# Kernel tuning notes

Measured on AMD Instinct MI355X. Metric: run time of the kernel, lower is better.

Reference implementation:

```python
import jax, jax.numpy as jnp
import numpy as np

TOKENS, D_MODEL, D_FF, RANK = 16384, 1024, 2816, 16


def setup_inputs() -> dict:
    key = jax.random.key(0)
    ks = jax.random.split(key, 7)
    s = lambda k, shp, scale: jax.random.normal(k, shp, dtype=jnp.float32) * scale
    return {
        "x": s(ks[0], (TOKENS, D_MODEL), 1.0),
        "W_gate_up": s(ks[1], (D_MODEL, 2 * D_FF), 0.02),
        "A_gate_up": s(ks[2], (D_MODEL, RANK), 0.02),
        "B_gate_up": s(ks[3], (RANK, 2 * D_FF), 0.02),
        "W_down": s(ks[4], (D_FF, D_MODEL), 0.02),
        "A_down": s(ks[5], (D_FF, RANK), 0.02),
        "B_down": s(ks[6], (RANK, D_MODEL), 0.02),
    }


def reference(x, W_gate_up, A_gate_up, B_gate_up, W_down, A_down, B_down):
    # gate_up_proj: base GEMM + LoRA low-rank correction
    gate_up = x @ W_gate_up + (x @ A_gate_up) @ B_gate_up  # [T, 2*D_FF]
    gate, up = jnp.split(gate_up, 2, axis=-1)
    h = jax.nn.silu(gate) * up  # SiluAndMul, [T, D_FF]
    # down_proj: base GEMM + LoRA correction
    out = h @ W_down + (h @ A_down) @ B_down  # [T, D_MODEL]
    return out
```

## Files before the change

### kernel.cpp

```cpp
#include <hip/hip_runtime.h>


typedef __bf16 bf16_t;
typedef __bf16 bf16x4 __attribute__((ext_vector_type(4)));
typedef __bf16 bf16x8 __attribute__((ext_vector_type(8)));
typedef float f32x4 __attribute__((ext_vector_type(4)));

#define TOKENS 16384
#define DMODEL 1024
#define DFF    2816
#define N2F    5632

#define BARM() asm volatile("s_barrier" ::: "memory")
#define VMW(n) asm volatile("s_waitcnt vmcnt(" #n ")" ::: "memory")
#define MFMA(d, va, vb) d = __builtin_amdgcn_mfma_f32_16x16x32_bf16(va, vb, d, 0, 0, 0)

__device__ __forceinline__ void gload16(const bf16_t* g, bf16_t* l) {
    __builtin_amdgcn_global_load_lds(
        (const __attribute__((address_space(1))) void*)g,
        (__attribute__((address_space(3))) void*)l, 16, 0, 0);
}

template<int KTOT, int NTOT>
__global__ __launch_bounds__(256) void prep_weff(
        const float* __restrict__ W, const float* __restrict__ A,
        const float* __restrict__ B, bf16_t* __restrict__ Wt) {
    __shared__ float Ws[64][65];
    __shared__ float As[64][17];
    __shared__ float Bs[16][64];
    const int t = threadIdx.x;
    const int k0 = blockIdx.x * 64, n0 = blockIdx.y * 64;
    #pragma unroll
    for (int i = 0; i < 16; ++i) {
        int row = i * 4 + t / 64, col = t % 64;
        Ws[row][col] = W[(size_t)(k0 + row) * NTOT + n0 + col];
    }
    #pragma unroll
    for (int i = 0; i < 4; ++i) {
        int idx = i * 256 + t;
        As[idx / 16][idx % 16] = A[(size_t)(k0 + idx / 16) * 16 + idx % 16];
    }
    #pragma unroll
    for (int i = 0; i < 4; ++i) {
        int idx = i * 256 + t;
        Bs[idx / 64][idx % 64] = B[(size_t)(idx / 64) * NTOT + n0 + idx % 64];
    }
    __syncthreads();
    const int kl = t % 64;
    #pragma unroll
    for (int j = 0; j < 16; ++j) {
        int nl = j * 4 + t / 64;
        float val = Ws[kl][nl];
        #pragma unroll
        for (int r = 0; r < 16; ++r) val += As[kl][r] * Bs[r][nl];
        Wt[(size_t)(n0 + nl) * KTOT + k0 + kl] = (bf16_t)val;
    }
}

__global__ __launch_bounds__(256) void conv_bf16(
        const float* __restrict__ in, bf16_t* __restrict__ out, int n4) {
    int i = blockIdx.x * 256 + threadIdx.x;
    if (i < n4) {
        float4 v = ((const float4*)in)[i];
        bf16x4 o;
        o.x = (bf16_t)v.x; o.y = (bf16_t)v.y; o.z = (bf16_t)v.z; o.w = (bf16_t)v.w;
        ((bf16x4*)out)[i] = o;
    }
}

__global__ __launch_bounds__(512, 2) void gemm1(
        const bf16_t* __restrict__ X, const bf16_t* __restrict__ Wt,
        bf16_t* __restrict__ H) {
    __shared__ bf16_t lds[65536];
    const int t = threadIdx.x, l = t & 63;
    const int wid = t >> 6, wr = wid >> 2, wc = wid & 3;
    const int l15 = l & 15, lhi = l >> 4;
    const int wg = ((int)blockIdx.x & 7) * 176 + ((int)blockIdx.x >> 3);
    const int tf = wg >> 6, tm = wg & 63;
    const int mbase = tm * 256, fbase = tf * 128;
    const int srow = t >> 2;
    const int sc8 = (((t & 3) ^ (srow & 3))) * 8;
    const bf16_t* gA  = X  + (size_t)(mbase + srow) * DMODEL + sc8;
    const bf16_t* gBg = Wt + (size_t)(fbase + srow) * DMODEL + sc8;
    const bf16_t* gBu = Wt + (size_t)(DFF + fbase + srow) * DMODEL + sc8;
    bf16_t* sdA = lds + wid * 512;
    bf16_t* sdB = lds + 16384 + wid * 512;
    const int aoff = (wr * 128 + l15) * 32 + (lhi ^ (l15 & 3)) * 8;
    const int boff = 16384 + (wc * 32 + l15) * 32 + (lhi ^ (l15 & 3)) * 8;

    f32x4 accg[8][2] = {}, accu[8][2] = {};
    bf16x8 a[4], bg[2], bu[2];

#define G1_STAGE_A(kt, ks, buf) do { const int kc = (kt) * 64 + (ks) * 32;        \
    gload16(gA + kc, sdA + (buf) * 32768 + (ks) * 8192);                          \
    gload16(gA + (size_t)128 * DMODEL + kc,                                       \
            sdA + (buf) * 32768 + (ks) * 8192 + 4096); } while (0)
#define G1_STAGE_B(kt, ks, buf) do { const int kc = (kt) * 64 + (ks) * 32;        \
    gload16(gBg + kc, sdB + (buf) * 32768 + (ks) * 8192);                         \
    gload16(gBu + kc, sdB + (buf) * 32768 + (ks) * 8192 + 4096); } while (0)
#define G1_READ_A(mh, ks, cur) do {                                               \
    const bf16_t* p = lds + (cur) * 32768 + (ks) * 8192 + (mh) * 2048 + aoff;     \
    a[0] = *(const bf16x8*)(p);        a[1] = *(const bf16x8*)(p + 512);          \
    a[2] = *(const bf16x8*)(p + 1024); a[3] = *(const bf16x8*)(p + 1536); } while (0)
#define G1_READ_B(ks, cur) do {                                                   \
    const bf16_t* p = lds + (cur) * 32768 + (ks) * 8192 + boff;                   \
    bg[0] = *(const bf16x8*)(p);        bg[1] = *(const bf16x8*)(p + 512);        \
    bu[0] = *(const bf16x8*)(p + 4096); bu[1] = *(const bf16x8*)(p + 4608); } while (0)
#define G1_MFMA(mh) do { __builtin_amdgcn_s_setprio(1);                           \
    _Pragma("unroll")                                                             \
    for (int i = 0; i < 4; ++i) {                                                 \
        MFMA(accg[(mh) * 4 + i][0], a[i], bg[0]);                                 \
        MFMA(accu[(mh) * 4 + i][0], a[i], bu[0]);                                 \
        MFMA(accg[(mh) * 4 + i][1], a[i], bg[1]);                                 \
        MFMA(accu[(mh) * 4 + i][1], a[i], bu[1]);                                 \
    }                                                                             \
    __builtin_amdgcn_s_setprio(0); } while (0)

    G1_STAGE_A(0, 0, 0); G1_STAGE_B(0, 0, 0); G1_STAGE_A(0, 1, 0); G1_STAGE_B(0, 1, 0);
    G1_STAGE_B(1, 0, 1); G1_STAGE_A(1, 0, 1); G1_STAGE_B(1, 1, 1);
    VMW(6); BARM();

    const int NT = DMODEL / 64;
    for (int kt = 0; kt < NT; ++kt) {
        const int cur = kt & 1, nxt = cur ^ 1;
        if (kt + 1 < NT) G1_STAGE_A(kt + 1, 1, nxt);
        G1_READ_A(0, 0, cur); G1_READ_B(0, cur);
        BARM();
        G1_MFMA(0);
        BARM();
        if (kt + 2 < NT) G1_STAGE_B(kt + 2, 0, cur);
        G1_READ_A(1, 0, cur);
        BARM();
        G1_MFMA(1);
        BARM();
        if (kt + 2 < NT) G1_STAGE_A(kt + 2, 0, cur);
        G1_READ_A(0, 1, cur); G1_READ_B(1, cur);
        BARM();
        G1_MFMA(0);
        BARM();
        if (kt + 2 < NT) G1_STAGE_B(kt + 2, 1, cur);
        G1_READ_A(1, 1, cur);
        if (kt + 2 < NT) { VMW(6); } else { VMW(0); }
        BARM();
        G1_MFMA(1);
        BARM();
    }
#undef G1_STAGE_A
#undef G1_STAGE_B
#undef G1_READ_A
#undef G1_READ_B
#undef G1_MFMA

    #pragma unroll
    for (int m = 0; m < 8; ++m)
        #pragma unroll
        for (int n = 0; n < 2; ++n)
            #pragma unroll
            for (int r = 0; r < 4; ++r) {
                int row = mbase + wr * 128 + m * 16 + lhi * 4 + r;
                int col = fbase + wc * 32 + n * 16 + l15;
                float g = accg[m][n][r], u = accu[m][n][r];
                H[(size_t)row * DFF + col] = (bf16_t)(g / (1.0f + __expf(-g)) * u);
            }
}

__global__ __launch_bounds__(512, 2) void gemm2(
        const bf16_t* __restrict__ Hm, const bf16_t* __restrict__ Wt,
        float* __restrict__ O) {
    __shared__ bf16_t lds[65536];
    const int t = threadIdx.x, l = t & 63;
    const int wid = t >> 6, wr = wid >> 2, wc = wid & 3;
    const int l15 = l & 15, lhi = l >> 4;
    const int wg = ((int)blockIdx.x & 7) * 32 + ((int)blockIdx.x >> 3);
    const int tn = wg >> 6, tm = wg & 63;
    const int mbase = tm * 256, nbase = tn * 256;
    const int srow = t >> 2;
    const int sc8 = (((t & 3) ^ (srow & 3))) * 8;
    const bf16_t* gA = Hm + (size_t)(mbase + srow) * DFF + sc8;
    const bf16_t* gB = Wt + (size_t)(nbase + srow) * DFF + sc8;
    bf16_t* sdA = lds + wid * 512;
    bf16_t* sdB = lds + 16384 + wid * 512;
    const int aoff = (wr * 128 + l15) * 32 + (lhi ^ (l15 & 3)) * 8;
    const int boff = 16384 + (wc * 64 + l15) * 32 + (lhi ^ (l15 & 3)) * 8;

    f32x4 acc[8][4] = {};
    bf16x8 a[4], b[4];

#define G2_STAGE_A(kt, ks, buf) do { const int kc = (kt) * 64 + (ks) * 32;        \
    gload16(gA + kc, sdA + (buf) * 32768 + (ks) * 8192);                          \
    gload16(gA + (size_t)128 * DFF + kc,                                          \
            sdA + (buf) * 32768 + (ks) * 8192 + 4096); } while (0)
#define G2_STAGE_B(kt, ks, buf) do { const int kc = (kt) * 64 + (ks) * 32;        \
    gload16(gB + kc, sdB + (buf) * 32768 + (ks) * 8192);                          \
    gload16(gB + (size_t)128 * DFF + kc,                                          \
            sdB + (buf) * 32768 + (ks) * 8192 + 4096); } while (0)
#define G2_READ_A(mh, ks, cur) do {                                               \
    const bf16_t* p = lds + (cur) * 32768 + (ks) * 8192 + (mh) * 2048 + aoff;     \
    a[0] = *(const bf16x8*)(p);        a[1] = *(const bf16x8*)(p + 512);          \
    a[2] = *(const bf16x8*)(p + 1024); a[3] = *(const bf16x8*)(p + 1536); } while (0)
#define G2_READ_B(ks, cur) do {                                                   \
    const bf16_t* p = lds + (cur) * 32768 + (ks) * 8192 + boff;                   \
    b[0] = *(const bf16x8*)(p);        b[1] = *(const bf16x8*)(p + 512);          \
    b[2] = *(const bf16x8*)(p + 1024); b[3] = *(const bf16x8*)(p + 1536); } while (0)
#define G2_MFMA(mh) do { __builtin_amdgcn_s_setprio(1);                           \
    _Pragma("unroll")                                                             \
    for (int i = 0; i < 4; ++i) {                                                 \
        MFMA(acc[(mh) * 4 + i][0], a[i], b[0]);                                   \
        MFMA(acc[(mh) * 4 + i][1], a[i], b[1]);                                   \
        MFMA(acc[(mh) * 4 + i][2], a[i], b[2]);                                   \
        MFMA(acc[(mh) * 4 + i][3], a[i], b[3]);                                   \
    }                                                                             \
    __builtin_amdgcn_s_setprio(0); } while (0)

    G2_STAGE_A(0, 0, 0); G2_STAGE_B(0, 0, 0); G2_STAGE_A(0, 1, 0); G2_STAGE_B(0, 1, 0);
    G2_STAGE_B(1, 0, 1); G2_STAGE_A(1, 0, 1); G2_STAGE_B(1, 1, 1);
    VMW(6); BARM();

    const int NT = DFF / 64;
    for (int kt = 0; kt < NT; ++kt) {
        const int cur = kt & 1, nxt = cur ^ 1;
        if (kt + 1 < NT) G2_STAGE_A(kt + 1, 1, nxt);
        G2_READ_A(0, 0, cur); G2_READ_B(0, cur);
        BARM();
        G2_MFMA(0);
        BARM();
        if (kt + 2 < NT) G2_STAGE_B(kt + 2, 0, cur);
        G2_READ_A(1, 0, cur);
        BARM();
        G2_MFMA(1);
        BARM();
        if (kt + 2 < NT) G2_STAGE_A(kt + 2, 0, cur);
        G2_READ_A(0, 1, cur); G2_READ_B(1, cur);
        BARM();
        G2_MFMA(0);
        BARM();
        if (kt + 2 < NT) G2_STAGE_B(kt + 2, 1, cur);
        G2_READ_A(1, 1, cur);
        if (kt + 2 < NT) { VMW(6); } else { VMW(0); }
        BARM();
        G2_MFMA(1);
        BARM();
    }
#undef G2_STAGE_A
#undef G2_STAGE_B
#undef G2_READ_A
#undef G2_READ_B
#undef G2_MFMA

    #pragma unroll
    for (int m = 0; m < 8; ++m)
        #pragma unroll
        for (int n = 0; n < 4; ++n)
            #pragma unroll
            for (int r = 0; r < 4; ++r) {
                int row = mbase + wr * 128 + m * 16 + lhi * 4 + r;
                int col = nbase + wc * 64 + n * 16 + l15;
                O[(size_t)row * DMODEL + col] = acc[m][n][r];
            }
}

extern "C" void kernel_launch(void* const* d_in, const int* in_sizes, int n_in,
                              void* d_out, int out_size, void* d_ws, size_t ws_size,
                              hipStream_t stream) {
    const float* x   = (const float*)d_in[0];
    const float* Wgu = (const float*)d_in[1];
    const float* Agu = (const float*)d_in[2];
    const float* Bgu = (const float*)d_in[3];
    const float* Wd  = (const float*)d_in[4];
    const float* Ad  = (const float*)d_in[5];
    const float* Bd  = (const float*)d_in[6];
    float* out = (float*)d_out;
    char* ws = (char*)d_ws;

    bf16_t* wgut = (bf16_t*)(ws);
    bf16_t* wdt  = (bf16_t*)(ws + 11534336);
    bf16_t* xb   = (bf16_t*)(ws + 17301504);
    bf16_t* hb   = (bf16_t*)(ws + 50855936);

    prep_weff<DMODEL, N2F><<<dim3(DMODEL / 64, N2F / 64), 256, 0, stream>>>(
        Wgu, Agu, Bgu, wgut);
    prep_weff<DFF, DMODEL><<<dim3(DFF / 64, DMODEL / 64), 256, 0, stream>>>(
        Wd, Ad, Bd, wdt);
    conv_bf16<<<(TOKENS * DMODEL / 4) / 256, 256, 0, stream>>>(
        x, xb, TOKENS * DMODEL / 4);
    gemm1<<<22 * 64, 512, 0, stream>>>(xb, wgut, hb);
    gemm2<<<4 * 64, 512, 0, stream>>>(hb, wdt, out);
}
```

Baseline: 369.8 us.

## Shrink GEMM tiles and switch to triple-buffered single-barrier K pipeline

Both GEMMs move from 256x128 (gemm1) and 256x256 (gemm2) tiles with a double-buffered, 64-wide K step and eight barriers per iteration to half-width tiles with a 32-wide K step, three LDS buffers and two barriers per iteration. LDS per block drops and launch bounds rise to 4 blocks per CU, which doubles the grid and aims for more occupancy and better latency hiding. The trade-off is lower arithmetic intensity per tile: there are fewer MFMAs per LDS read and more global traffic for re-reading the shared operand.

After: 411.4 us. +11.2%, slower.

```diff
diff --git a/kernel.cpp b/kernel.cpp
--- a/kernel.cpp
+++ b/kernel.cpp
@@ -68,192 +68,149 @@
     }
 }
 
-__global__ __launch_bounds__(512, 2) void gemm1(
+__global__ __launch_bounds__(512, 4) void gemm1(
         const bf16_t* __restrict__ X, const bf16_t* __restrict__ Wt,
         bf16_t* __restrict__ H) {
-    __shared__ bf16_t lds[65536];
+    __shared__ bf16_t lds[36864];
     const int t = threadIdx.x, l = t & 63;
-    const int wid = t >> 6, wr = wid >> 2, wc = wid & 3;
+    const int wid = t >> 6, wr = wid >> 1, wc = wid & 1;
     const int l15 = l & 15, lhi = l >> 4;
-    const int wg = ((int)blockIdx.x & 7) * 176 + ((int)blockIdx.x >> 3);
+    const int wg = ((int)blockIdx.x & 7) * 352 + ((int)blockIdx.x >> 3);
     const int tf = wg >> 6, tm = wg & 63;
-    const int mbase = tm * 256, fbase = tf * 128;
+    const int mbase = tm * 256, fbase = tf * 64;
     const int srow = t >> 2;
-    const int sc8 = (((t & 3) ^ (srow & 3))) * 8;
-    const bf16_t* gA  = X  + (size_t)(mbase + srow) * DMODEL + sc8;
-    const bf16_t* gBg = Wt + (size_t)(fbase + srow) * DMODEL + sc8;
-    const bf16_t* gBu = Wt + (size_t)(DFF + fbase + srow) * DMODEL + sc8;
+    const int sc8 = ((t & 3) ^ (srow & 3)) * 8;
+    const bf16_t* gA  = X + (size_t)(mbase + srow) * DMODEL + sc8;
+    const bf16_t* gA2 = gA + (size_t)128 * DMODEL;
+    const int brow = (srow < 64) ? (fbase + srow) : (DFF + fbase + srow - 64);
+    const bf16_t* gB  = Wt + (size_t)brow * DMODEL + sc8;
     bf16_t* sdA = lds + wid * 512;
-    bf16_t* sdB = lds + 16384 + wid * 512;
-    const int aoff = (wr * 128 + l15) * 32 + (lhi ^ (l15 & 3)) * 8;
-    const int boff = 16384 + (wc * 32 + l15) * 32 + (lhi ^ (l15 & 3)) * 8;
-
-    f32x4 accg[8][2] = {}, accu[8][2] = {};
+    bf16_t* sdB = lds + 8192 + wid * 512;
+    const int rsw = (lhi ^ (l15 & 3)) * 8;
+    const int aoff = (wr * 64 + l15) * 32 + rsw;
+    const int boff = 8192 + (wc * 32 + l15) * 32 + rsw;
+
+    f32x4 accg[4][2] = {}, accu[4][2] = {};
     bf16x8 a[4], bg[2], bu[2];
 
-#define G1_STAGE_A(kt, ks, buf) do { const int kc = (kt) * 64 + (ks) * 32;        \
-    gload16(gA + kc, sdA + (buf) * 32768 + (ks) * 8192);                          \
-    gload16(gA + (size_t)128 * DMODEL + kc,                                       \
-            sdA + (buf) * 32768 + (ks) * 8192 + 4096); } while (0)
-#define G1_STAGE_B(kt, ks, buf) do { const int kc = (kt) * 64 + (ks) * 32;        \
-    gload16(gBg + kc, sdB + (buf) * 32768 + (ks) * 8192);                         \
-    gload16(gBu + kc, sdB + (buf) * 32768 + (ks) * 8192 + 4096); } while (0)
-#define G1_READ_A(mh, ks, cur) do {                                               \
-    const bf16_t* p = lds + (cur) * 32768 + (ks) * 8192 + (mh) * 2048 + aoff;     \
+#define G1_STAGE(kt, buf) do { const int kc = (kt) * 32;                          \
+    bf16_t* d = (buf) * 12288 + sdA;                                              \
+    gload16(gA + kc, d); gload16(gA2 + kc, d + 4096);                             \
+    gload16(gB + kc, (buf) * 12288 + sdB); } while (0)
+#define G1_READ(buf) do {                                                         \
+    const bf16_t* p = lds + (buf) * 12288 + aoff;                                 \
     a[0] = *(const bf16x8*)(p);        a[1] = *(const bf16x8*)(p + 512);          \
-    a[2] = *(const bf16x8*)(p + 1024); a[3] = *(const bf16x8*)(p + 1536); } while (0)
-#define G1_READ_B(ks, cur) do {                                                   \
-    const bf16_t* p = lds + (cur) * 32768 + (ks) * 8192 + boff;                   \
-    bg[0] = *(const bf16x8*)(p);        bg[1] = *(const bf16x8*)(p + 512);        \
-    bu[0] = *(const bf16x8*)(p + 4096); bu[1] = *(const bf16x8*)(p + 4608); } while (0)
-#define G1_MFMA(mh) do { __builtin_amdgcn_s_setprio(1);                           \
+    a[2] = *(const bf16x8*)(p + 1024); a[3] = *(const bf16x8*)(p + 1536);         \
+    const bf16_t* q = lds + (buf) * 12288 + boff;                                 \
+    bg[0] = *(const bf16x8*)(q);        bg[1] = *(const bf16x8*)(q + 512);        \
+    bu[0] = *(const bf16x8*)(q + 2048); bu[1] = *(const bf16x8*)(q + 2560); } while (0)
+#define G1_MFMA() do { __builtin_amdgcn_s_setprio(1);                             \
     _Pragma("unroll")                                                             \
     for (int i = 0; i < 4; ++i) {                                                 \
-        MFMA(accg[(mh) * 4 + i][0], a[i], bg[0]);                                 \
-        MFMA(accu[(mh) * 4 + i][0], a[i], bu[0]);                                 \
-        MFMA(accg[(mh) * 4 + i][1], a[i], bg[1]);                                 \
-        MFMA(accu[(mh) * 4 + i][1], a[i], bu[1]);                                 \
+        MFMA(accg[i][0], a[i], bg[0]); MFMA(accu[i][0], a[i], bu[0]);             \
+        MFMA(accg[i][1], a[i], bg[1]); MFMA(accu[i][1], a[i], bu[1]);             \
     }                                                                             \
     __builtin_amdgcn_s_setprio(0); } while (0)
 
-    G1_STAGE_A(0, 0, 0); G1_STAGE_B(0, 0, 0); G1_STAGE_A(0, 1, 0); G1_STAGE_B(0, 1, 0);
-    G1_STAGE_B(1, 0, 1); G1_STAGE_A(1, 0, 1); G1_STAGE_B(1, 1, 1);
+    const int NT = DMODEL / 32;
+    G1_STAGE(0, 0); G1_STAGE(1, 1); G1_STAGE(2, 2);
     VMW(6); BARM();
-
-    const int NT = DMODEL / 64;
+    int buf = 0;
     for (int kt = 0; kt < NT; ++kt) {
-        const int cur = kt & 1, nxt = cur ^ 1;
-        if (kt + 1 < NT) G1_STAGE_A(kt + 1, 1, nxt);
-        G1_READ_A(0, 0, cur); G1_READ_B(0, cur);
-        BARM();
-        G1_MFMA(0);
-        BARM();
-        if (kt + 2 < NT) G1_STAGE_B(kt + 2, 0, cur);
-        G1_READ_A(1, 0, cur);
-        BARM();
-        G1_MFMA(1);
-        BARM();
-        if (kt + 2 < NT) G1_STAGE_A(kt + 2, 0, cur);
-        G1_READ_A(0, 1, cur); G1_READ_B(1, cur);
-        BARM();
-        G1_MFMA(0);
-        BARM();
-        if (kt + 2 < NT) G1_STAGE_B(kt + 2, 1, cur);
-        G1_READ_A(1, 1, cur);
-        if (kt + 2 < NT) { VMW(6); } else { VMW(0); }
-        BARM();
-        G1_MFMA(1);
-        BARM();
-    }
-#undef G1_STAGE_A
-#undef G1_STAGE_B
-#undef G1_READ_A
-#undef G1_READ_B
+        G1_READ(buf);
+        G1_MFMA();
+        BARM();
+        if (kt + 3 < NT) { G1_STAGE(kt + 3, buf); VMW(6); }
+        else if (kt == NT - 3) { VMW(3); }
+        else if (kt == NT - 2) { VMW(0); }
+        BARM();
+        buf = (buf == 2) ? 0 : buf + 1;
+    }
+#undef G1_STAGE
+#undef G1_READ
 #undef G1_MFMA
 
     #pragma unroll
-    for (int m = 0; m < 8; ++m)
+    for (int m = 0; m < 4; ++m)
         #pragma unroll
         for (int n = 0; n < 2; ++n)
             #pragma unroll
             for (int r = 0; r < 4; ++r) {
-                int row = mbase + wr * 128 + m * 16 + lhi * 4 + r;
+                int row = mbase + wr * 64 + m * 16 + lhi * 4 + r;
                 int col = fbase + wc * 32 + n * 16 + l15;
                 float g = accg[m][n][r], u = accu[m][n][r];
                 H[(size_t)row * DFF + col] = (bf16_t)(g / (1.0f + __expf(-g)) * u);
             }
 }
 
-__global__ __launch_bounds__(512, 2) void gemm2(
+__global__ __launch_bounds__(512, 4) void gemm2(
         const bf16_t* __restrict__ Hm, const bf16_t* __restrict__ Wt,
         float* __restrict__ O) {
-    __shared__ bf16_t lds[65536];
+    __shared__ bf16_t lds[36864];
     const int t = threadIdx.x, l = t & 63;
-    const int wid = t >> 6, wr = wid >> 2, wc = wid & 3;
+    const int wid = t >> 6, wr = wid >> 1, wc = wid & 1;
     const int l15 = l & 15, lhi = l >> 4;
-    const int wg = ((int)blockIdx.x & 7) * 32 + ((int)blockIdx.x >> 3);
+    const int wg = ((int)blockIdx.x & 7) * 64 + ((int)blockIdx.x >> 3);
     const int tn = wg >> 6, tm = wg & 63;
-    const int mbase = tm * 256, nbase = tn * 256;
+    const int mbase = tm * 256, nbase = tn * 128;
     const int srow = t >> 2;
-    const int sc8 = (((t & 3) ^ (srow & 3))) * 8;
-    const bf16_t* gA = Hm + (size_t)(mbase + srow) * DFF + sc8;
-    const bf16_t* gB = Wt + (size_t)(nbase + srow) * DFF + sc8;
+    const int sc8 = ((t & 3) ^ (srow & 3)) * 8;
+    const bf16_t* gA  = Hm + (size_t)(mbase + srow) * DFF + sc8;
+    const bf16_t* gA2 = gA + (size_t)128 * DFF;
+    const bf16_t* gB  = Wt + (size_t)(nbase + srow) * DFF + sc8;
     bf16_t* sdA = lds + wid * 512;
-    bf16_t* sdB = lds + 16384 + wid * 512;
-    const int aoff = (wr * 128 + l15) * 32 + (lhi ^ (l15 & 3)) * 8;
-    const int boff = 16384 + (wc * 64 + l15) * 32 + (lhi ^ (l15 & 3)) * 8;
-
-    f32x4 acc[8][4] = {};
+    bf16_t* sdB = lds + 8192 + wid * 512;
+    const int rsw = (lhi ^ (l15 & 3)) * 8;
+    const int aoff = (wr * 64 + l15) * 32 + rsw;
+    const int boff = 8192 + (wc * 64 + l15) * 32 + rsw;
+
+    f32x4 acc[4][4] = {};
     bf16x8 a[4], b[4];
 
-#define G2_STAGE_A(kt, ks, buf) do { const int kc = (kt) * 64 + (ks) * 32;        \
-    gload16(gA + kc, sdA + (buf) * 32768 + (ks) * 8192);                          \
-    gload16(gA + (size_t)128 * DFF + kc,                                          \
-            sdA + (buf) * 32768 + (ks) * 8192 + 4096); } while (0)
-#define G2_STAGE_B(kt, ks, buf) do { const int kc = (kt) * 64 + (ks) * 32;        \
-    gload16(gB + kc, sdB + (buf) * 32768 + (ks) * 8192);                          \
-    gload16(gB + (size_t)128 * DFF + kc,                                          \
-            sdB + (buf) * 32768 + (ks) * 8192 + 4096); } while (0)
-#define G2_READ_A(mh, ks, cur) do {                                               \
-    const bf16_t* p = lds + (cur) * 32768 + (ks) * 8192 + (mh) * 2048 + aoff;     \
+#define G2_STAGE(kt, buf) do { const int kc = (kt) * 32;                          \
+    bf16_t* d = (buf) * 12288 + sdA;                                              \
+    gload16(gA + kc, d); gload16(gA2 + kc, d + 4096);                             \
+    gload16(gB + kc, (buf) * 12288 + sdB); } while (0)
+#define G2_READ(buf) do {                                                         \
+    const bf16_t* p = lds + (buf) * 12288 + aoff;                                 \
     a[0] = *(const bf16x8*)(p);        a[1] = *(const bf16x8*)(p + 512);          \
-    a[2] = *(const bf16x8*)(p + 1024); a[3] = *(const bf16x8*)(p + 1536); } while (0)
-#define G2_READ_B(ks, cur) do {                                                   \
-    const bf16_t* p = lds + (cur) * 32768 + (ks) * 8192 + boff;                   \
-    b[0] = *(const bf16x8*)(p);        b[1] = *(const bf16x8*)(p + 512);          \
-    b[2] = *(const bf16x8*)(p + 1024); b[3] = *(const bf16x8*)(p + 1536); } while (0)
-#define G2_MFMA(mh) do { __builtin_amdgcn_s_setprio(1);                           \
+    a[2] = *(const bf16x8*)(p + 1024); a[3] = *(const bf16x8*)(p + 1536);         \
+    const bf16_t* q = lds + (buf) * 12288 + boff;                                 \
+    b[0] = *(const bf16x8*)(q);        b[1] = *(const bf16x8*)(q + 512);          \
+    b[2] = *(const bf16x8*)(q + 1024); b[3] = *(const bf16x8*)(q + 1536); } while (0)
+#define G2_MFMA() do { __builtin_amdgcn_s_setprio(1);                             \
     _Pragma("unroll")                                                             \
     for (int i = 0; i < 4; ++i) {                                                 \
-        MFMA(acc[(mh) * 4 + i][0], a[i], b[0]);                                   \
-        MFMA(acc[(mh) * 4 + i][1], a[i], b[1]);                                   \
-        MFMA(acc[(mh) * 4 + i][2], a[i], b[2]);                                   \
-        MFMA(acc[(mh) * 4 + i][3], a[i], b[3]);                                   \
+        MFMA(acc[i][0], a[i], b[0]); MFMA(acc[i][1], a[i], b[1]);                 \
+        MFMA(acc[i][2], a[i], b[2]); MFMA(acc[i][3], a[i], b[3]);                 \
     }                                                                             \
     __builtin_amdgcn_s_setprio(0); } while (0)
 
-    G2_STAGE_A(0, 0, 0); G2_STAGE_B(0, 0, 0); G2_STAGE_A(0, 1, 0); G2_STAGE_B(0, 1, 0);
-    G2_STAGE_B(1, 0, 1); G2_STAGE_A(1, 0, 1); G2_STAGE_B(1, 1, 1);
+    const int NT = DFF / 32;
+    G2_STAGE(0, 0); G2_STAGE(1, 1); G2_STAGE(2, 2);
     VMW(6); BARM();
-
-    const int NT = DFF / 64;
+    int buf = 0;
     for (int kt = 0; kt < NT; ++kt) {
-        const int cur = kt & 1, nxt = cur ^ 1;
-        if (kt + 1 < NT) G2_STAGE_A(kt + 1, 1, nxt);
-        G2_READ_A(0, 0, cur); G2_READ_B(0, cur);
-        BARM();
-        G2_MFMA(0);
-        BARM();
-        if (kt + 2 < NT) G2_STAGE_B(kt + 2, 0, cur);
-        G2_READ_A(1, 0, cur);
-        BARM();
-        G2_MFMA(1);
-        BARM();
-        if (kt + 2 < NT) G2_STAGE_A(kt + 2, 0, cur);
-        G2_READ_A(0, 1, cur); G2_READ_B(1, cur);
-        BARM();
-        G2_MFMA(0);
-        BARM();
-        if (kt + 2 < NT) G2_STAGE_B(kt + 2, 1, cur);
-        G2_READ_A(1, 1, cur);
-        if (kt + 2 < NT) { VMW(6); } else { VMW(0); }
-        BARM();
-        G2_MFMA(1);
-        BARM();
-    }
-#undef G2_STAGE_A
-#undef G2_STAGE_B
-#undef G2_READ_A
-#undef G2_READ_B
+        G2_READ(buf);
+        G2_MFMA();
+        BARM();
+        if (kt + 3 < NT) { G2_STAGE(kt + 3, buf); VMW(6); }
+        else if (kt == NT - 3) { VMW(3); }
+        else if (kt == NT - 2) { VMW(0); }
+        BARM();
+        buf = (buf == 2) ? 0 : buf + 1;
+    }
+#undef G2_STAGE
+#undef G2_READ
 #undef G2_MFMA
 
     #pragma unroll
-    for (int m = 0; m < 8; ++m)
+    for (int m = 0; m < 4; ++m)
         #pragma unroll
         for (int n = 0; n < 4; ++n)
             #pragma unroll
             for (int r = 0; r < 4; ++r) {
-                int row = mbase + wr * 128 + m * 16 + lhi * 4 + r;
+                int row = mbase + wr * 64 + m * 16 + lhi * 4 + r;
                 int col = nbase + wc * 64 + n * 16 + l15;
                 O[(size_t)row * DMODEL + col] = acc[m][n][r];
             }
@@ -283,6 +240,6 @@
         Wd, Ad, Bd, wdt);
     conv_bf16<<<(TOKENS * DMODEL / 4) / 256, 256, 0, stream>>>(
         x, xb, TOKENS * DMODEL / 4);
-    gemm1<<<22 * 64, 512, 0, stream>>>(xb, wgut, hb);
-    gemm2<<<4 * 64, 512, 0, stream>>>(hb, wdt, out);
-}
+    gemm1<<<44 * 64, 512, 0, stream>>>(xb, wgut, hb);
+    gemm2<<<8 * 64, 512, 0, stream>>>(hb, wdt, out);
+}
```
